# Performance work log

Measured on AMD Instinct MI355X. Metric: run time of the kernel, lower is better.

Reference implementation:

```python
import jax, jax.numpy as jnp
import numpy as np

NUM_NODES = 50000
NUM_RELS = 256
D = 256            # node_in_feat
TEXT_D = 256       # text_emb_dim
T_TOTAL = 24       # number of unique timestep graphs
E = 20000          # edges per timestep graph
B = 16             # batch of query times
SEQ_LEN = 7


def setup_inputs() -> dict:
    key = jax.random.key(0)
    ks = jax.random.split(key, 12)
    s = 1.0 / np.sqrt(D)
    return {
        "node_embeds": jax.random.normal(ks[0], (NUM_NODES, D), jnp.float32),
        "text_emb": jax.random.normal(ks[1], (T_TOTAL, E, TEXT_D), jnp.float32),
        "text_w_W": jax.random.uniform(ks[2], (TEXT_D, D), jnp.float32, -s, s),
        "text_w_b": jax.random.uniform(ks[3], (D,), jnp.float32, -s, s),
        "edge_w_W": jax.random.uniform(ks[4], (3 * D, D), jnp.float32, -s, s),
        "edge_w_b": jax.random.uniform(ks[5], (D,), jnp.float32, -s, s),
        "gru_Wih": jax.random.uniform(ks[6], (D, 3 * D), jnp.float32, -s, s),
        "gru_Whh": jax.random.uniform(ks[7], (D, 3 * D), jnp.float32, -s, s),
        "gru_bih": jax.random.uniform(ks[8], (3 * D,), jnp.float32, -s, s),
        "gru_bhh": jax.random.uniform(ks[9], (3 * D,), jnp.float32, -s, s),
        "edge_src": jax.random.randint(ks[10], (T_TOTAL, E), 0, NUM_NODES, jnp.int32),
        "edge_dst": jax.random.randint(jax.random.fold_in(ks[10], 1), (T_TOTAL, E), 0, NUM_NODES, jnp.int32),
        "edge_rel": jax.random.randint(jax.random.fold_in(ks[10], 2), (T_TOTAL, E), 0, NUM_RELS, jnp.int32),
        "time_idx": jax.random.randint(ks[11], (B, SEQ_LEN), 0, T_TOTAL, jnp.int32),
    }


def _gru(seqs, Wih, Whh, bih, bhh):
    # seqs: [B, R, S, d] -> run GRU over S, return final hidden [B, R, d]
    xs = jnp.moveaxis(seqs, 2, 0)  # [S, B, R, d]
    h0 = jnp.zeros(seqs.shape[:2] + (seqs.shape[-1],), seqs.dtype)

    def step(h, x):
        gi = x @ Wih + bih            # [B, R, 3d]
        gh = h @ Whh + bhh
        i_r, i_z, i_n = jnp.split(gi, 3, axis=-1)
        h_r, h_z, h_n = jnp.split(gh, 3, axis=-1)
        r = jax.nn.sigmoid(i_r + h_r)
        z = jax.nn.sigmoid(i_z + h_z)
        n = jnp.tanh(i_n + r * h_n)
        h_new = (1.0 - z) * n + z * h
        return h_new, None

    h_final, _ = jax.lax.scan(step, h0, xs)
    return h_final


def reference(node_embeds, text_emb, text_w_W, text_w_b, edge_w_W, edge_w_b,
              gru_Wih, gru_Whh, gru_bih, gru_bhh,
              edge_src, edge_dst, edge_rel, time_idx):
    # edge text projection (text_w): [T, E, D]
    text_h = text_emb @ text_w_W + text_w_b
    # gather node embeddings per edge endpoint
    h_src = node_embeds[edge_src]  # [T, E, D]
    h_dst = node_embeds[edge_dst]  # [T, E, D]
    # concat + edge MLP + ReLU: e_h = relu(edge_w([src || text || dst]))
    e = jnp.concatenate([h_src, text_h, h_dst], axis=-1)  # [T, E, 3D]
    e_h = jax.nn.relu(e @ edge_w_W + edge_w_b)            # [T, E, D]

    # scatter-mean of edge embeddings by relation type per timestep graph;
    # relations absent in a graph get zeros (init_rel_embeds = zeros)
    seg = lambda v, r: jax.ops.segment_sum(v, r, num_segments=NUM_RELS)
    sums = jax.vmap(seg)(e_h, edge_rel)                               # [T, R, D]
    counts = jax.vmap(seg)(jnp.ones(edge_rel.shape, e_h.dtype), edge_rel)  # [T, R]
    counts = counts[..., None]
    rel_emb = jnp.where(counts > 0, sums / jnp.maximum(counts, 1.0), 0.0)  # [T, R, D]

    # per query time: gather its window of timestep rel-embeddings and run
    # the GRU over time (relations act as the GRU batch dim, like transpose(0,1))
    seqs = rel_emb[time_idx]                 # [B, S, R, D]
    seqs = jnp.swapaxes(seqs, 1, 2)          # [B, R, S, D]
    hn = _gru(seqs, gru_Wih, gru_Whh, gru_bih, gru_bhh)  # [B, R, D]
    return hn
```

## Files before the change

### kernel.cpp

```cpp
#include <hip/hip_runtime.h>
#include <cstdint>
#include <cstddef>

#define NNODES 50000
#define NPAD   50048
#define NRELS  256
#define DIM    256
#define TT     24
#define EE     20000
#define BATCH  16
#define SEQQ   7

typedef __bf16 bf16;
typedef __bf16 bf16x4 __attribute__((ext_vector_type(4)));
typedef __bf16 bf16x8 __attribute__((ext_vector_type(8)));
typedef float  f32x4  __attribute__((ext_vector_type(4)));

__device__ __forceinline__ void gload16(const void* g, void* l){
  __builtin_amdgcn_global_load_lds((const __attribute__((address_space(1))) void*)g,
                                   (__attribute__((address_space(3))) void*)l, 16, 0, 0);
}


__global__ void k_cvt8(const float* __restrict__ in, bf16* __restrict__ out, int n8){
  int i = blockIdx.x*256 + threadIdx.x;
  if (i >= n8) return;
  const float4* p = (const float4*)in + (size_t)i*2;
  float4 a = p[0], b = p[1];
  bf16x8 o;
  o[0]=(bf16)a.x; o[1]=(bf16)a.y; o[2]=(bf16)a.z; o[3]=(bf16)a.w;
  o[4]=(bf16)b.x; o[5]=(bf16)b.y; o[6]=(bf16)b.z; o[7]=(bf16)b.w;
  ((bf16x8*)out)[i] = o;
}

__global__ void k_build_wbt(const float* __restrict__ tW, const float* __restrict__ eW,
                            bf16* __restrict__ WbT){
  int n = blockIdx.x, j = threadIdx.x;
  WbT[(size_t)n*768 + j]       = (bf16)eW[(size_t)j*256 + n];
  WbT[(size_t)n*768 + 512 + j] = (bf16)eW[(size_t)(512+j)*256 + n];
  float acc = 0.f;
  for (int m=0; m<256; ++m) acc += tW[(size_t)j*256 + m] * eW[(size_t)(256+m)*256 + n];
  WbT[(size_t)n*768 + 256 + j] = (bf16)acc;
}

__global__ void k_bias(const float* __restrict__ tb, const float* __restrict__ eW,
                       const float* __restrict__ eb, float* __restrict__ bf){
  int n = threadIdx.x;
  float acc = eb[n];
  for (int m=0; m<256; ++m) acc += tb[m] * eW[(size_t)(256+m)*256 + n];
  bf[n] = acc;
}

__global__ void k_gruWT(const float* __restrict__ W, bf16* __restrict__ WT){
  int n = blockIdx.x, k = threadIdx.x;
  WT[(size_t)n*256 + k] = (bf16)W[(size_t)k*768 + n];
}

__global__ void k_hist(const int* __restrict__ rel, int* __restrict__ counts,
                       int* __restrict__ offs, int* __restrict__ cursor){
  __shared__ int hist[256];
  __shared__ int scan[256];
  int t = blockIdx.x, tid = threadIdx.x;
  hist[tid] = 0;
  __syncthreads();
  for (int e = tid; e < EE; e += 256) atomicAdd(&hist[rel[(size_t)t*EE + e]], 1);
  __syncthreads();
  int v = hist[tid];
  scan[tid] = v;
  __syncthreads();
  for (int d=1; d<256; d<<=1){
    int add = (tid >= d) ? scan[tid-d] : 0;
    __syncthreads();
    scan[tid] += add;
    __syncthreads();
  }
  int ex = scan[tid] - v;
  counts[t*256+tid] = v;
  offs[t*256+tid]   = ex;
  cursor[t*256+tid] = ex;
}

__global__ void k_perm(const int* __restrict__ rel, const int* __restrict__ esrc,
                       const int* __restrict__ edst, int* __restrict__ cursor,
                       int* __restrict__ gperm, int* __restrict__ src_p,
                       int* __restrict__ dst_p){
  int t = blockIdx.y;
  int e = blockIdx.x*256 + threadIdx.x;
  if (e < EE){
    int r = rel[(size_t)t*EE + e];
    int p = atomicAdd(&cursor[t*256 + r], 1);
    size_t g = (size_t)t*EE + p;
    gperm[g] = t*EE + e;
    src_p[g] = esrc[(size_t)t*EE + e];
    dst_p[g] = edst[(size_t)t*EE + e];
  }
}

__global__ __launch_bounds__(256) void k_projn(
    const bf16* __restrict__ Abf, const bf16* __restrict__ WbT, int koff,
    bf16* __restrict__ out)
{
  int m0 = blockIdx.x*128;
  int tid = threadIdx.x, lane = tid&63, w = tid>>6;
  int l15 = lane&15, lq = lane>>4;
  int c0 = w*64;
  __shared__ __align__(16) bf16 Al[128*32];
  __shared__ __align__(16) bf16 Bl[256*32];

  f32x4 acc[8][4];
  f32x4 z4 = {0.f,0.f,0.f,0.f};
  #pragma unroll
  for (int mi=0;mi<8;++mi)
    #pragma unroll
    for (int ni=0;ni<4;++ni) acc[mi][ni]=z4;

  for (int ks=0; ks<8; ++ks){
    int k0 = ks*32;
    #pragma unroll
    for (int p=0;p<2;++p){
      int c = p*256 + tid;
      int rw = c>>2, prt = c&3;
      int pp = prt ^ ((rw>>1)&3);
      const char* src = (const char*)(Abf + (size_t)(m0+rw)*256 + k0) + pp*16;
      gload16(src, (char*)Al + (size_t)(p*256 + w*64)*16);
    }
    #pragma unroll
    for (int p=0;p<4;++p){
      int c = p*256 + tid;
      int nn = c>>2, prt = c&3;
      int pp = prt ^ ((nn>>1)&3);
      const char* src = (const char*)(WbT + (size_t)nn*768 + koff + k0) + pp*16;
      gload16(src, (char*)Bl + (size_t)(p*256 + w*64)*16);
    }
    __syncthreads();
    bf16x8 b[4];
    #pragma unroll
    for (int ni=0;ni<4;++ni){
      int nn = c0 + ni*16 + l15;
      b[ni] = *(const bf16x8*)((const char*)Bl + (size_t)nn*64 + (size_t)((lq ^ ((nn>>1)&3))*16));
    }
    #pragma unroll
    for (int mi=0;mi<8;++mi){
      int rw = mi*16 + l15;
      bf16x8 a = *(const bf16x8*)((const char*)Al + (size_t)rw*64 + (size_t)((lq ^ ((rw>>1)&3))*16));
      #pragma unroll
      for (int ni=0;ni<4;++ni)
        acc[mi][ni] = __builtin_amdgcn_mfma_f32_16x16x32_bf16(b[ni], a, acc[mi][ni], 0,0,0);
    }
    __syncthreads();
  }
  #pragma unroll
  for (int mi=0;mi<8;++mi){
    int row = m0 + mi*16 + l15;
    #pragma unroll
    for (int ni=0;ni<4;++ni){
      bf16x4 o;
      #pragma unroll
      for (int q=0;q<4;++q) o[q] = (bf16)acc[mi][ni][q];
      *(bf16x4*)(out + (size_t)row*256 + c0 + ni*16 + lq*4) = o;
    }
  }
}

__global__ __launch_bounds__(256,4) void k_projt(
    const float* __restrict__ text, const int* __restrict__ gperm,
    const bf16* __restrict__ WbT, bf16* __restrict__ out)
{
  int m0 = blockIdx.x*64;
  int tid = threadIdx.x, lane = tid&63, w = tid>>6;
  int l15 = lane&15, lq = lane>>4;
  int c0 = w*64;
  __shared__ __align__(16) float Afl[2][64*32];
  __shared__ __align__(16) bf16  Bl[2][256*32];

  int rA0 = tid>>3;
  int partA = tid&7;
  int ppA = partA ^ (rA0 & 7);
  const float* aPtr0 = text + (size_t)gperm[m0 + rA0]*256      + ppA*4;
  const float* aPtr1 = text + (size_t)gperm[m0 + 32 + rA0]*256 + ppA*4;

#define STAGEA(KS, BI)                                                        \
  { gload16(aPtr0 + (KS)*32, (char*)&Afl[BI][0] + (size_t)(w*64)*16);         \
    gload16(aPtr1 + (KS)*32, (char*)&Afl[BI][0] + (size_t)(256 + w*64)*16); }

#define STAGEB(KS, BI)                                                        \
  { _Pragma("unroll")                                                         \
    for (int p_=0;p_<4;++p_){                                                 \
      int c_ = p_*256 + tid;                                                  \
      int nn_ = c_>>2, prt_ = c_&3;                                           \
      int pp_ = prt_ ^ ((nn_>>1)&3);                                          \
      const char* src_ = (const char*)(WbT + (size_t)nn_*768 + 256 + (KS)*32) + pp_*16; \
      gload16(src_, (char*)&Bl[BI][0] + (size_t)(p_*256 + w*64)*16); } }

  f32x4 acc[4][4];
  f32x4 z4 = {0.f,0.f,0.f,0.f};
  #pragma unroll
  for (int mi=0;mi<4;++mi)
    #pragma unroll
    for (int ni=0;ni<4;++ni) acc[mi][ni]=z4;

  STAGEA(0, 0);
  STAGEB(0, 0);

  #pragma unroll
  for (int ks=0; ks<8; ++ks){
    const int bi = ks & 1;
    if (ks < 7){
      STAGEA(ks+1, bi^1);
      STAGEB(ks+1, bi^1);
      asm volatile("s_waitcnt vmcnt(6)\n\ts_barrier" ::: "memory");
    } else {
      asm volatile("s_waitcnt vmcnt(0)\n\ts_barrier" ::: "memory");
    }
    __builtin_amdgcn_sched_barrier(0);
    bf16x8 a[4], b[4];
    #pragma unroll
    for (int ni=0;ni<4;++ni){
      int nn = c0 + ni*16 + l15;
      b[ni] = *(const bf16x8*)((const char*)&Bl[bi][0]
               + (size_t)nn*64 + (size_t)((lq ^ ((nn>>1)&3))*16));
    }
    #pragma unroll
    for (int mi=0;mi<4;++mi){
      int rw = mi*16 + l15;
      int sw = l15 & 7;
      const char* ab = (const char*)&Afl[bi][0] + (size_t)rw*128;
      f32x4 f0 = *(const f32x4*)(ab + (size_t)(((lq*2+0)^sw))*16);
      f32x4 f1 = *(const f32x4*)(ab + (size_t)(((lq*2+1)^sw))*16);
      bf16x8 o;
      o[0]=(bf16)f0[0]; o[1]=(bf16)f0[1]; o[2]=(bf16)f0[2]; o[3]=(bf16)f0[3];
      o[4]=(bf16)f1[0]; o[5]=(bf16)f1[1]; o[6]=(bf16)f1[2]; o[7]=(bf16)f1[3];
      a[mi] = o;
    }
    asm volatile("s_waitcnt lgkmcnt(0)" ::: "memory");
    __builtin_amdgcn_sched_barrier(0);
    #pragma unroll
    for (int mi=0;mi<4;++mi)
      #pragma unroll
      for (int ni=0;ni<4;++ni)
        acc[mi][ni] = __builtin_amdgcn_mfma_f32_16x16x32_bf16(b[ni], a[mi], acc[mi][ni], 0,0,0);
    if (ks < 7)
      __builtin_amdgcn_s_barrier();
  }
#undef STAGEA
#undef STAGEB

  #pragma unroll
  for (int mi=0;mi<4;++mi){
    int row = m0 + mi*16 + l15;
    #pragma unroll
    for (int ni=0;ni<4;++ni){
      bf16x4 o;
      #pragma unroll
      for (int q=0;q<4;++q) o[q] = (bf16)acc[mi][ni][q];
      *(bf16x4*)(out + (size_t)row*256 + c0 + ni*16 + lq*4) = o;
    }
  }
}

__global__ __launch_bounds__(256) void k_comb(
    const bf16* __restrict__ P, const bf16* __restrict__ Q,
    const bf16* __restrict__ T, const float* __restrict__ bfused,
    const int* __restrict__ src_p, const int* __restrict__ dst_p,
    const int* __restrict__ counts, const int* __restrict__ offs,
    bf16* __restrict__ rel_bf)
{
  int r = blockIdx.x, t = blockIdx.y;
  int tid = threadIdx.x;
  int tr = t*256 + r;
  int nE = counts[tr];
  if (nE == 0){
    rel_bf[(size_t)tr*256 + tid] = (bf16)0.f;
    return;
  }
  int base = offs[tr];
  int es = tid>>5, cg = (tid&31)*8;
  float bb[8];
  {
    float4 b0 = *(const float4*)(bfused + cg);
    float4 b1 = *(const float4*)(bfused + cg + 4);
    bb[0]=b0.x; bb[1]=b0.y; bb[2]=b0.z; bb[3]=b0.w;
    bb[4]=b1.x; bb[5]=b1.y; bb[6]=b1.z; bb[7]=b1.w;
  }
  float acc[8];
  #pragma unroll
  for (int j=0;j<8;++j) acc[j]=0.f;
  for (int i = es; i < nE; i += 8){
    size_t g = (size_t)t*EE + base + i;
    int s = src_p[g], d = dst_p[g];
    bf16x8 pv = *(const bf16x8*)(P + (size_t)s*256 + cg);
    bf16x8 qv = *(const bf16x8*)(Q + (size_t)d*256 + cg);
    bf16x8 tv = *(const bf16x8*)(T + g*256 + cg);
    #pragma unroll
    for (int j=0;j<8;++j)
      acc[j] += fmaxf((float)pv[j] + (float)qv[j] + (float)tv[j] + bb[j], 0.f);
  }
  __shared__ float red[8][256];
  #pragma unroll
  for (int j=0;j<8;++j) red[es][cg+j] = acc[j];
  __syncthreads();
  float s = 0.f;
  #pragma unroll
  for (int e=0;e<8;++e) s += red[e][tid];
  rel_bf[(size_t)tr*256 + tid] = (bf16)(s / (float)nE);
}

__global__ __launch_bounds__(256) void k_gemm(
    const bf16* __restrict__ A, const bf16* __restrict__ BT,
    const float* __restrict__ bias, float* __restrict__ Out)
{
  int m0 = blockIdx.x*128, n0 = blockIdx.y*128;
  int tid = threadIdx.x, lane = tid&63, w = tid>>6;
  int l15 = lane&15, lq = lane>>4;
  __shared__ __align__(16) bf16 Al[128*32];
  __shared__ __align__(16) bf16 Bl[128*32];
  int wr = (w&1)*64, wc = (w>>1)*64;
  f32x4 acc[4][4];
  f32x4 z4 = {0.f,0.f,0.f,0.f};
  #pragma unroll
  for (int mi=0;mi<4;++mi)
    #pragma unroll
    for (int ni=0;ni<4;++ni) acc[mi][ni]=z4;
  for (int ks=0; ks<8; ++ks){
    int k0 = ks*32;
    #pragma unroll
    for (int p=0;p<2;++p){
      int c = p*256 + tid;
      int rw = c>>2, part = c&3;
      int pp = part ^ ((rw>>1)&3);
      const char* src = (const char*)(A + (size_t)(m0+rw)*256 + k0) + pp*16;
      gload16(src, (char*)Al + (size_t)(p*256 + w*64)*16);
    }
    #pragma unroll
    for (int p=0;p<2;++p){
      int c = p*256 + tid;
      int nn = c>>2, part = c&3;
      int pp = part ^ ((nn>>1)&3);
      const char* src = (const char*)(BT + (size_t)(n0+nn)*256 + k0) + pp*16;
      gload16(src, (char*)Bl + (size_t)(p*256 + w*64)*16);
    }
    __syncthreads();
    bf16x8 a[4], b[4];
    #pragma unroll
    for (int mi=0;mi<4;++mi){
      int rw = wr + mi*16 + l15;
      a[mi] = *(const bf16x8*)((const char*)Al + (size_t)rw*64 + (size_t)((lq ^ ((rw>>1)&3))*16));
    }
    #pragma unroll
    for (int ni=0;ni<4;++ni){
      int nn = wc + ni*16 + l15;
      b[ni] = *(const bf16x8*)((const char*)Bl + (size_t)nn*64 + (size_t)((lq ^ ((nn>>1)&3))*16));
    }
    #pragma unroll
    for (int mi=0;mi<4;++mi)
      #pragma unroll
      for (int ni=0;ni<4;++ni)
        acc[mi][ni] = __builtin_amdgcn_mfma_f32_16x16x32_bf16(a[mi], b[ni], acc[mi][ni], 0,0,0);
    __syncthreads();
  }
  #pragma unroll
  for (int ni=0;ni<4;++ni){
    int col = n0 + wc + ni*16 + l15;
    float bv = bias[col];
    #pragma unroll
    for (int mi=0;mi<4;++mi){
      #pragma unroll
      for (int q=0;q<4;++q){
        int row = m0 + wr + mi*16 + lq*4 + q;
        Out[(size_t)row*768 + col] = acc[mi][ni][q] + bv;
      }
    }
  }
}

__global__ __launch_bounds__(256) void k_gru(
    const float* __restrict__ GI, const bf16* __restrict__ WhhT,
    const float* __restrict__ bhh, const int* __restrict__ time_idx,
    float* __restrict__ out)
{
  int blk = blockIdx.x;
  int tid = threadIdx.x, lane = tid&63, w = tid>>6;
  int l15 = lane&15, lq = lane>>4;
  int b = blk >> 4;
  int rr = ((blk & 15)*16) + l15;
  __shared__ __align__(16) bf16 Ah[16*256];

  f32x4 h[4];
  #pragma unroll
  for (int jq=0;jq<4;++jq) h[jq] = f32x4{0.f,0.f,0.f,0.f};

  for (int s=0; s<SEQQ; ++s){
    int t = time_idx[b*SEQQ + s];
    size_t gib = (size_t)(t*256 + rr)*768;
    f32x4 gh[12];
    #pragma unroll
    for (int ni=0;ni<12;++ni){
      int col = (ni>>2)*256 + w*64 + (ni&3)*16 + lq*4;
      gh[ni] = *(const f32x4*)(bhh + col);
    }
    if (s > 0){
      #pragma unroll
      for (int ks=0; ks<8; ++ks){
        bf16x8 a = *(const bf16x8*)(&Ah[0] + (size_t)l15*256 + ks*32 + lq*8);
        #pragma unroll
        for (int ni=0;ni<12;++ni){
          int n = (ni>>2)*256 + w*64 + (ni&3)*16 + l15;
          bf16x8 wv = *(const bf16x8*)(WhhT + (size_t)n*256 + ks*32 + lq*8);
          gh[ni] = __builtin_amdgcn_mfma_f32_16x16x32_bf16(wv, a, gh[ni], 0,0,0);
        }
      }
    }
    #pragma unroll
    for (int jq=0;jq<4;++jq){
      int col = w*64 + jq*16 + lq*4;
      f32x4 ir = *(const f32x4*)(GI + gib + col);
      f32x4 iz = *(const f32x4*)(GI + gib + 256 + col);
      f32x4 in = *(const f32x4*)(GI + gib + 512 + col);
      #pragma unroll
      for (int q=0;q<4;++q){
        float rg = 1.f/(1.f + __expf(-(ir[q] + gh[jq][q])));
        float zz = 1.f/(1.f + __expf(-(iz[q] + gh[4+jq][q])));
        float nn = tanhf(in[q] + rg*gh[8+jq][q]);
        h[jq][q] = (1.f - zz)*nn + zz*h[jq][q];
      }
    }
    if (s < SEQQ-1){
      __syncthreads();
      #pragma unroll
      for (int jq=0;jq<4;++jq){
        bf16x4 o;
        #pragma unroll
        for (int q=0;q<4;++q) o[q] = (bf16)h[jq][q];
        *(bf16x4*)(&Ah[0] + (size_t)l15*256 + w*64 + jq*16 + lq*4) = o;
      }
      __syncthreads();
    }
  }
  #pragma unroll
  for (int jq=0;jq<4;++jq){
    f32x4 o = h[jq];
    *(f32x4*)(out + (size_t)(blk*16 + l15)*256 + w*64 + jq*16 + lq*4) = o;
  }
}

extern "C" void kernel_launch(void* const* d_in, const int* in_sizes, int n_in,
                              void* d_out, int out_size, void* d_ws, size_t ws_size,
                              hipStream_t stream)
{
  (void)in_sizes; (void)n_in; (void)out_size; (void)ws_size;
  const float* node_embeds = (const float*)d_in[0];
  const float* text_emb    = (const float*)d_in[1];
  const float* text_w_W    = (const float*)d_in[2];
  const float* text_w_b    = (const float*)d_in[3];
  const float* edge_w_W    = (const float*)d_in[4];
  const float* edge_w_b    = (const float*)d_in[5];
  const float* gru_Wih     = (const float*)d_in[6];
  const float* gru_Whh     = (const float*)d_in[7];
  const float* gru_bih     = (const float*)d_in[8];
  const float* gru_bhh     = (const float*)d_in[9];
  const int* edge_src      = (const int*)d_in[10];
  const int* edge_dst      = (const int*)d_in[11];
  const int* edge_rel      = (const int*)d_in[12];
  const int* time_idx      = (const int*)d_in[13];
  float* out = (float*)d_out;
  char* ws = (char*)d_ws;

  size_t o = 0;
  bf16*  WbT    = (bf16*) (ws + o); o += (size_t)768*256*2;
  bf16*  WihT   = (bf16*) (ws + o); o += (size_t)768*256*2;
  bf16*  WhhT   = (bf16*) (ws + o); o += (size_t)768*256*2;
  float* bfused = (float*)(ws + o); o += 1024;
  bf16*  node_bf= (bf16*) (ws + o); o += (size_t)NPAD*256*2;
  int*   counts = (int*)  (ws + o); o += (size_t)TT*256*4;
  int*   offs   = (int*)  (ws + o); o += (size_t)TT*256*4;
  int*   cursor = (int*)  (ws + o); o += (size_t)TT*256*4;
  int*   gperm  = (int*)  (ws + o); o += (size_t)TT*EE*4;
  int*   src_p  = (int*)  (ws + o); o += (size_t)TT*EE*4;
  int*   dst_p  = (int*)  (ws + o); o += (size_t)TT*EE*4;
  bf16*  rel_bf = (bf16*) (ws + o); o += (size_t)TT*256*256*2;
  bf16*  P      = (bf16*) (ws + o); o += (size_t)NPAD*256*2;
  bf16*  Q      = (bf16*) (ws + o); o += (size_t)NPAD*256*2;
  size_t oT = o;
  bf16*  Tproj  = (bf16*) (ws + oT);
  float* GI     = (float*)(ws + oT);

  k_cvt8<<<6250,256,0,stream>>>(node_embeds, node_bf, NNODES*256/8);
  k_build_wbt<<<256,256,0,stream>>>(text_w_W, edge_w_W, WbT);
  k_bias<<<1,256,0,stream>>>(text_w_b, edge_w_W, edge_w_b, bfused);
  k_gruWT<<<768,256,0,stream>>>(gru_Wih, WihT);
  k_gruWT<<<768,256,0,stream>>>(gru_Whh, WhhT);
  k_hist<<<TT,256,0,stream>>>(edge_rel, counts, offs, cursor);
  k_perm<<<dim3((EE+255)/256,TT),256,0,stream>>>(edge_rel, edge_src, edge_dst,
                                                 cursor, gperm, src_p, dst_p);
  k_projn<<<NPAD/128,256,0,stream>>>(node_bf, WbT, 0,   P);
  k_projn<<<NPAD/128,256,0,stream>>>(node_bf, WbT, 512, Q);
  k_projt<<<TT*EE/64,256,0,stream>>>(text_emb, gperm, WbT, Tproj);
  k_comb<<<dim3(256,TT),256,0,stream>>>(P, Q, Tproj, bfused, src_p, dst_p,
                                        counts, offs, rel_bf);
  k_gemm<<<dim3(48,6),256,0,stream>>>(rel_bf, WihT, gru_bih, GI);
  k_gru<<<256,256,0,stream>>>(GI, WhhT, gru_bhh, time_idx, out);
}
```

Baseline: 585.0 us.

## Fuse edge combine, ReLU and per-relation reduction into text projection GEMM epilogue

The text projection GEMM now adds the gathered P/Q node projections and the bias, applies ReLU in registers, and reduces rows by relation run with cross-lane shuffles and float atomics into a zeroed rel_sum buffer. A small mean kernel then divides by counts. This removes the bf16 Tproj intermediate write and re-read and the separate combine kernel. The cost is extra epilogue work, atomic contention at relation-run boundaries, a memset, lower occupancy from the launch bounds change, and a serial run scan done by one thread.

```diff
diff --git a/kernel.cpp b/kernel.cpp
--- a/kernel.cpp
+++ b/kernel.cpp
@@ -83,7 +83,7 @@
 __global__ void k_perm(const int* __restrict__ rel, const int* __restrict__ esrc,
                        const int* __restrict__ edst, int* __restrict__ cursor,
                        int* __restrict__ gperm, int* __restrict__ src_p,
-                       int* __restrict__ dst_p){
+                       int* __restrict__ dst_p, int* __restrict__ tr_p){
   int t = blockIdx.y;
   int e = blockIdx.x*256 + threadIdx.x;
   if (e < EE){
@@ -93,6 +93,7 @@
     gperm[g] = t*EE + e;
     src_p[g] = esrc[(size_t)t*EE + e];
     dst_p[g] = edst[(size_t)t*EE + e];
+    tr_p[g]  = t*256 + r;
   }
 }
 
@@ -162,9 +163,12 @@
   }
 }
 
-__global__ __launch_bounds__(256,4) void k_projt(
+__global__ __launch_bounds__(256,3) void k_projtc(
     const float* __restrict__ text, const int* __restrict__ gperm,
-    const bf16* __restrict__ WbT, bf16* __restrict__ out)
+    const bf16* __restrict__ WbT, const float* __restrict__ bfused,
+    const bf16* __restrict__ P, const bf16* __restrict__ Q,
+    const int* __restrict__ src_p, const int* __restrict__ dst_p,
+    const int* __restrict__ tr_p, float* __restrict__ rel_sum)
 {
   int m0 = blockIdx.x*64;
   int tid = threadIdx.x, lane = tid&63, w = tid>>6;
@@ -172,6 +176,25 @@
   int c0 = w*64;
   __shared__ __align__(16) float Afl[2][64*32];
   __shared__ __align__(16) bf16  Bl[2][256*32];
+  __shared__ int trA[64], sIl[64], dIl[64];
+  __shared__ int runS[65], runT[64];
+  __shared__ int nRunS;
+
+  if (tid < 64){
+    int g = m0 + tid;
+    trA[tid] = tr_p[g];
+    sIl[tid] = src_p[g];
+    dIl[tid] = dst_p[g];
+  }
+  __syncthreads();
+  if (tid == 0){
+    int nR = 0;
+    for (int i=0;i<64;++i){
+      if (i==0 || trA[i]!=trA[i-1]){ runS[nR]=i; runT[nR]=trA[i]; ++nR; }
+    }
+    runS[nR] = 64;
+    nRunS = nR;
+  }
 
   int rA0 = tid>>3;
   int partA = tid&7;
@@ -245,64 +268,63 @@
 #undef STAGEA
 #undef STAGEB
 
+  float4 bias4[4];
+  #pragma unroll
+  for (int ni=0;ni<4;++ni)
+    bias4[ni] = *(const float4*)(bfused + c0 + ni*16 + lq*4);
+
   #pragma unroll
   for (int mi=0;mi<4;++mi){
-    int row = m0 + mi*16 + l15;
+    int row = mi*16 + l15;
+    int srow = sIl[row], drow = dIl[row];
     #pragma unroll
     for (int ni=0;ni<4;++ni){
-      bf16x4 o;
-      #pragma unroll
-      for (int q=0;q<4;++q) o[q] = (bf16)acc[mi][ni][q];
-      *(bf16x4*)(out + (size_t)row*256 + c0 + ni*16 + lq*4) = o;
-    }
-  }
-}
-
-__global__ __launch_bounds__(256) void k_comb(
-    const bf16* __restrict__ P, const bf16* __restrict__ Q,
-    const bf16* __restrict__ T, const float* __restrict__ bfused,
-    const int* __restrict__ src_p, const int* __restrict__ dst_p,
-    const int* __restrict__ counts, const int* __restrict__ offs,
-    bf16* __restrict__ rel_bf)
-{
-  int r = blockIdx.x, t = blockIdx.y;
-  int tid = threadIdx.x;
-  int tr = t*256 + r;
-  int nE = counts[tr];
-  if (nE == 0){
-    rel_bf[(size_t)tr*256 + tid] = (bf16)0.f;
-    return;
-  }
-  int base = offs[tr];
-  int es = tid>>5, cg = (tid&31)*8;
-  float bb[8];
-  {
-    float4 b0 = *(const float4*)(bfused + cg);
-    float4 b1 = *(const float4*)(bfused + cg + 4);
-    bb[0]=b0.x; bb[1]=b0.y; bb[2]=b0.z; bb[3]=b0.w;
-    bb[4]=b1.x; bb[5]=b1.y; bb[6]=b1.z; bb[7]=b1.w;
-  }
-  float acc[8];
-  #pragma unroll
-  for (int j=0;j<8;++j) acc[j]=0.f;
-  for (int i = es; i < nE; i += 8){
-    size_t g = (size_t)t*EE + base + i;
-    int s = src_p[g], d = dst_p[g];
-    bf16x8 pv = *(const bf16x8*)(P + (size_t)s*256 + cg);
-    bf16x8 qv = *(const bf16x8*)(Q + (size_t)d*256 + cg);
-    bf16x8 tv = *(const bf16x8*)(T + g*256 + cg);
-    #pragma unroll
-    for (int j=0;j<8;++j)
-      acc[j] += fmaxf((float)pv[j] + (float)qv[j] + (float)tv[j] + bb[j], 0.f);
-  }
-  __shared__ float red[8][256];
-  #pragma unroll
-  for (int j=0;j<8;++j) red[es][cg+j] = acc[j];
-  __syncthreads();
-  float s = 0.f;
-  #pragma unroll
-  for (int e=0;e<8;++e) s += red[e][tid];
-  rel_bf[(size_t)tr*256 + tid] = (bf16)(s / (float)nE);
+      bf16x4 pv = *(const bf16x4*)(P + (size_t)srow*256 + c0 + ni*16 + lq*4);
+      bf16x4 qv = *(const bf16x4*)(Q + (size_t)drow*256 + c0 + ni*16 + lq*4);
+      f32x4 t4 = acc[mi][ni];
+      t4[0] = fmaxf(t4[0] + (float)pv[0] + (float)qv[0] + bias4[ni].x, 0.f);
+      t4[1] = fmaxf(t4[1] + (float)pv[1] + (float)qv[1] + bias4[ni].y, 0.f);
+      t4[2] = fmaxf(t4[2] + (float)pv[2] + (float)qv[2] + bias4[ni].z, 0.f);
+      t4[3] = fmaxf(t4[3] + (float)pv[3] + (float)qv[3] + bias4[ni].w, 0.f);
+      acc[mi][ni] = t4;
+    }
+  }
+
+  int nR = nRunS;
+  for (int k=0; k<nR; ++k){
+    int rs = runS[k], re = runS[k+1], tr = runT[k];
+    float part16[16];
+    #pragma unroll
+    for (int ni=0;ni<4;++ni){
+      #pragma unroll
+      for (int q=0;q<4;++q){
+        float s = 0.f;
+        #pragma unroll
+        for (int mi=0;mi<4;++mi){
+          int row = mi*16 + l15;
+          s += (row >= rs && row < re) ? acc[mi][ni][q] : 0.f;
+        }
+        part16[ni*4+q] = s;
+      }
+    }
+    #pragma unroll
+    for (int m=1; m<16; m<<=1){
+      #pragma unroll
+      for (int s=0;s<16;++s) part16[s] += __shfl_xor(part16[s], m);
+    }
+    float v = part16[0];
+    #pragma unroll
+    for (int s=1;s<16;++s) v = (l15==s) ? part16[s] : v;
+    atomicAdd(&rel_sum[(size_t)tr*256 + c0 + ((l15>>2)<<4) + (lq<<2) + (l15&3)], v);
+  }
+}
+
+__global__ void k_mean(const float* __restrict__ rel_sum, const int* __restrict__ counts,
+                       bf16* __restrict__ rel_bf){
+  int tr = blockIdx.x, c = threadIdx.x;
+  int cnt = counts[tr];
+  float v = (cnt > 0) ? rel_sum[(size_t)tr*256 + c] / (float)cnt : 0.f;
+  rel_bf[(size_t)tr*256 + c] = (bf16)v;
 }
 
 __global__ __launch_bounds__(256) void k_gemm(
@@ -477,12 +499,12 @@
   int*   gperm  = (int*)  (ws + o); o += (size_t)TT*EE*4;
   int*   src_p  = (int*)  (ws + o); o += (size_t)TT*EE*4;
   int*   dst_p  = (int*)  (ws + o); o += (size_t)TT*EE*4;
+  int*   tr_p   = (int*)  (ws + o); o += (size_t)TT*EE*4;
   bf16*  rel_bf = (bf16*) (ws + o); o += (size_t)TT*256*256*2;
   bf16*  P      = (bf16*) (ws + o); o += (size_t)NPAD*256*2;
   bf16*  Q      = (bf16*) (ws + o); o += (size_t)NPAD*256*2;
-  size_t oT = o;
-  bf16*  Tproj  = (bf16*) (ws + oT);
-  float* GI     = (float*)(ws + oT);
+  float* rel_sum= (float*)(ws + o); o += (size_t)TT*256*256*4;
+  float* GI     = (float*)(ws + o); o += (size_t)TT*256*768*4;
 
   k_cvt8<<<6250,256,0,stream>>>(node_embeds, node_bf, NNODES*256/8);
   k_build_wbt<<<256,256,0,stream>>>(text_w_W, edge_w_W, WbT);
@@ -491,12 +513,13 @@
   k_gruWT<<<768,256,0,stream>>>(gru_Whh, WhhT);
   k_hist<<<TT,256,0,stream>>>(edge_rel, counts, offs, cursor);
   k_perm<<<dim3((EE+255)/256,TT),256,0,stream>>>(edge_rel, edge_src, edge_dst,
-                                                 cursor, gperm, src_p, dst_p);
+                                                 cursor, gperm, src_p, dst_p, tr_p);
   k_projn<<<NPAD/128,256,0,stream>>>(node_bf, WbT, 0,   P);
   k_projn<<<NPAD/128,256,0,stream>>>(node_bf, WbT, 512, Q);
-  k_projt<<<TT*EE/64,256,0,stream>>>(text_emb, gperm, WbT, Tproj);
-  k_comb<<<dim3(256,TT),256,0,stream>>>(P, Q, Tproj, bfused, src_p, dst_p,
-                                        counts, offs, rel_bf);
+  hipMemsetAsync(rel_sum, 0, (size_t)TT*256*256*4, stream);
+  k_projtc<<<TT*EE/64,256,0,stream>>>(text_emb, gperm, WbT, bfused, P, Q,
+                                      src_p, dst_p, tr_p, rel_sum);
+  k_mean<<<TT*256,256,0,stream>>>(rel_sum, counts, rel_bf);
   k_gemm<<<dim3(48,6),256,0,stream>>>(rel_bf, WihT, gru_bih, GI);
   k_gru<<<256,256,0,stream>>>(GI, WhhT, gru_bhh, time_idx, out);
 }
```

Measured after the change: 540.1 us, median of 2. -7.7%, faster.
